# Kernel optimization log

Measured on AMD Instinct MI355X. Metric: run time of the kernel, lower is better.

## Reference

```python
import jax, jax.numpy as jnp
import numpy as np

B, NPG = 128, 512            # graphs, nodes per graph (batch is contiguous & uniform)
N = B * NPG                  # 65536 nodes
DEG = 8
E = N * DEG                  # 524288 edges
F_IN, NHID = 128, 64
H, C = 3, NHID               # GAT heads, out channels per head
HC = H * C                   # 192
NCLS = 10
RATIO = 0.5
NEG_SLOPE = 0.2


def setup_inputs() -> dict:
    key = jax.random.key(0)
    ks = jax.random.split(key, 24)
    x = jax.random.normal(ks[0], (N, F_IN), jnp.float32)
    # edges constrained within each graph (graphs are contiguous blocks of NPG nodes)
    offs = jnp.repeat(jnp.arange(B, dtype=jnp.int32) * NPG, NPG * DEG)
    src = jax.random.randint(ks[1], (E,), 0, NPG, dtype=jnp.int32) + offs
    dst = jax.random.randint(ks[2], (E,), 0, NPG, dtype=jnp.int32) + offs
    edge_index = jnp.stack([src, dst], axis=0)
    edge_attr = jax.random.normal(ks[3], (E, 2), jnp.float32)
    batch = jnp.repeat(jnp.arange(B, dtype=jnp.int32), NPG)

    def lin(k, o, i):
        return jax.random.normal(k, (o, i), jnp.float32) / np.float32(np.sqrt(i))

    return {
        "x": x, "edge_index": edge_index, "edge_attr": edge_attr, "batch": batch,
        # lin: num_features -> nhid//2
        "W_lin": lin(ks[4], NHID // 2, F_IN), "b_lin": jnp.zeros((NHID // 2,), jnp.float32),
        # GATConv(nhid//2 -> nhid, heads=3, edge_dim=2)
        "W_src": lin(ks[5], HC, NHID // 2),
        "att_src": jax.random.normal(ks[6], (H, C), jnp.float32) / np.float32(np.sqrt(C)),
        "att_dst": jax.random.normal(ks[7], (H, C), jnp.float32) / np.float32(np.sqrt(C)),
        "W_edge": lin(ks[8], HC, 2),
        "att_edge": jax.random.normal(ks[9], (H, C), jnp.float32) / np.float32(np.sqrt(C)),
        "b_gat": jnp.zeros((HC,), jnp.float32),
        # SAGPool score layer: GCNConv(nhid*3 -> 1)
        "W_gcn": lin(ks[10], 1, HC), "b_gcn": jnp.zeros((1,), jnp.float32),
        # classifier MLP
        "W1": lin(ks[11], NHID, 2 * HC), "b1": jnp.zeros((NHID,), jnp.float32),
        "W2": lin(ks[12], NHID // 2, NHID), "b2": jnp.zeros((NHID // 2,), jnp.float32),
        "W3": lin(ks[13], NCLS, NHID // 2), "b3": jnp.zeros((NCLS,), jnp.float32),
    }


def reference(x, edge_index, edge_attr, batch,
              W_lin, b_lin, W_src, att_src, att_dst, W_edge, att_edge, b_gat,
              W_gcn, b_gcn, W1, b1, W2, b2, W3, b3):
    src, dst = edge_index[0], edge_index[1]

    # ---- lin + ELU -------------------------------------------------------
    h = jax.nn.elu(x @ W_lin.T + b_lin)                       # [N, nhid//2]

    # ---- GATConv(heads=3, edge_dim=2), add_self_loops fill_value='mean' --
    loop = jnp.arange(N, dtype=src.dtype)
    cnt = jax.ops.segment_sum(jnp.ones((E,), h.dtype), dst, num_segments=N)
    loop_attr = jax.ops.segment_sum(edge_attr, dst, num_segments=N) / jnp.maximum(cnt, 1.0)[:, None]
    s_full = jnp.concatenate([src, loop])
    d_full = jnp.concatenate([dst, loop])
    ea_full = jnp.concatenate([edge_attr, loop_attr], axis=0)  # [E+N, 2]

    xp = (h @ W_src.T).reshape(N, H, C)                        # projected per-head feats
    a_src = (xp * att_src).sum(-1)                             # [N, H]
    a_dst = (xp * att_dst).sum(-1)                             # [N, H]
    ef = (ea_full @ W_edge.T).reshape(-1, H, C)
    a_edge = (ef * att_edge).sum(-1)                           # [E+N, H]

    alpha = jax.nn.leaky_relu(a_src[s_full] + a_dst[d_full] + a_edge, NEG_SLOPE)
    m = jax.ops.segment_max(alpha, d_full, num_segments=N)     # scatter-softmax over dst
    ealpha = jnp.exp(alpha - m[d_full])
    denom = jax.ops.segment_sum(ealpha, d_full, num_segments=N)
    alpha = ealpha / (denom[d_full] + 1e-16)                   # [E+N, H]

    out = jax.ops.segment_sum(alpha[:, :, None] * xp[s_full], d_full, num_segments=N)
    x1 = jax.nn.relu(out.reshape(N, HC) + b_gat)               # [N, 192]

    # ---- SAGPool: GCNConv score + per-graph top-k (mask form) ------------
    xw = x1 @ W_gcn.T                                          # [N, 1]
    deg = jax.ops.segment_sum(jnp.ones((E,), x1.dtype), dst, num_segments=N) + 1.0
    dinv = jax.lax.rsqrt(deg)
    agg = jax.ops.segment_sum((dinv[src] * dinv[dst])[:, None] * xw[src], dst, num_segments=N)
    score = (agg + (dinv ** 2)[:, None] * xw + b_gcn)[:, 0]    # [N]

    k = int(np.ceil(RATIO * NPG))                              # nodes kept per graph
    s2 = score.reshape(B, NPG)
    rank = jnp.argsort(jnp.argsort(-s2, axis=1), axis=1)
    mask = rank < k                                            # [B, NPG] top-k selection

    xs = (x1 * jnp.tanh(score)[:, None]).reshape(B, NPG, HC)
    gmp = jnp.max(jnp.where(mask[:, :, None], xs, -jnp.inf), axis=1)   # [B, 192]
    gap = jnp.sum(jnp.where(mask[:, :, None], xs, 0.0), axis=1) / k    # [B, 192]
    r = jnp.concatenate([gmp, gap], axis=1)                    # [B, 384]

    # ---- classifier MLP (dropout is identity in eval) ---------------------
    r = jax.nn.relu(r @ W1.T + b1)
    r = jax.nn.relu(r @ W2.T + b2)
    return jax.nn.log_softmax(r @ W3.T + b3, axis=-1)          # [B, num_classes]
```

## Files before the change

kernel.cpp:

```cpp
#include <hip/hip_runtime.h>
#include <hip/hip_bf16.h>
#include <math.h>

#define NN   65536
#define EE   524288
#define BB   128
#define NPGC 512
#define HCC  192
#define KSEL 256
#define NEG  0.2f
#define PSEG 8
#define SEGN (NPGC / PSEG)
#define MAXD 40
#define SLOTS ((size_t)NN * MAXD)
#define EPG   4096

__device__ __forceinline__ int nodeblock_base(int bx) {
    int xcd = bx & 7, j = bx >> 3;
    int g = xcd + 8 * (j >> 1);
    return g * NPGC + (j & 1) * 256;
}

__global__ __launch_bounds__(192) void k_v(
    const float* __restrict__ W_src, const float* __restrict__ att_src,
    const float* __restrict__ att_dst, const float* __restrict__ W_edge,
    const float* __restrict__ att_edge, float* __restrict__ vbuf) {
    __shared__ float red[6];
    int t = threadIdx.x;
    if (t < 6) red[t] = 0.f;
    __syncthreads();
    {
        float ae = att_edge[t];
        int h = t >> 6;
        atomicAdd(&red[h],     W_edge[2 * t]     * ae);
        atomicAdd(&red[3 + h], W_edge[2 * t + 1] * ae);
    }
    if (t < 96) {
        int h = t >> 5, k = t & 31;
        float vs = 0.f, vd = 0.f;
        for (int c = 0; c < 64; ++c) {
            float w = W_src[(h * 64 + c) * 32 + k];
            vs += w * att_src[h * 64 + c];
            vd += w * att_dst[h * 64 + c];
        }
        vbuf[t] = vs;
        vbuf[96 + t] = vd;
    }
    __syncthreads();
    if (t < 6) vbuf[192 + t] = red[t];
}

__global__ __launch_bounds__(256) void k_h(
    const float* __restrict__ x, const float* __restrict__ W_lin,
    const float* __restrict__ b_lin, const float* __restrict__ vbuf,
    float* __restrict__ hbuf, float* __restrict__ ap_s, float* __restrict__ ap_d) {
    __shared__ float Wl[128 * 16];
    __shared__ float vs_s[48], vd_s[48];
    int t = threadIdx.x;
    int half = blockIdx.y;
#pragma unroll
    for (int i = 0; i < 8; ++i) {
        int idx = t + i * 256;
        int k = idx >> 4, jj = idx & 15;
        Wl[k * 16 + jj] = W_lin[(half * 16 + jj) * 128 + k];
    }
    if (t < 48) {
        int head = t >> 4, j = t & 15;
        vs_s[t] = vbuf[head * 32 + half * 16 + j];
        vd_s[t] = vbuf[96 + head * 32 + half * 16 + j];
    }
    __syncthreads();
    int g = (blockIdx.x & 7) + 8 * (blockIdx.x >> 3);
    int nA = g * NPGC + t, nB = nA + 256;
    const float4* xrA = (const float4*)(x + (size_t)nA * 128);
    const float4* xrB = (const float4*)(x + (size_t)nB * 128);
    float accA[16], accB[16];
#pragma unroll
    for (int j = 0; j < 16; ++j) {
        float bv = b_lin[half * 16 + j];
        accA[j] = bv; accB[j] = bv;
    }
#pragma unroll 2
    for (int q = 0; q < 32; ++q) {
        float4 xA = xrA[q], xB = xrB[q];
        const float4* w0 = (const float4*)&Wl[(q * 4 + 0) * 16];
        const float4* w1 = (const float4*)&Wl[(q * 4 + 1) * 16];
        const float4* w2 = (const float4*)&Wl[(q * 4 + 2) * 16];
        const float4* w3 = (const float4*)&Wl[(q * 4 + 3) * 16];
#pragma unroll
        for (int jq = 0; jq < 4; ++jq) {
            float4 a = w0[jq], b = w1[jq], c = w2[jq], d = w3[jq];
            accA[4*jq+0] += xA.x*a.x + xA.y*b.x + xA.z*c.x + xA.w*d.x;
            accA[4*jq+1] += xA.x*a.y + xA.y*b.y + xA.z*c.y + xA.w*d.y;
            accA[4*jq+2] += xA.x*a.z + xA.y*b.z + xA.z*c.z + xA.w*d.z;
            accA[4*jq+3] += xA.x*a.w + xA.y*b.w + xA.z*c.w + xA.w*d.w;
            accB[4*jq+0] += xB.x*a.x + xB.y*b.x + xB.z*c.x + xB.w*d.x;
            accB[4*jq+1] += xB.x*a.y + xB.y*b.y + xB.z*c.y + xB.w*d.y;
            accB[4*jq+2] += xB.x*a.z + xB.y*b.z + xB.z*c.z + xB.w*d.z;
            accB[4*jq+3] += xB.x*a.w + xB.y*b.w + xB.z*c.w + xB.w*d.w;
        }
    }
#pragma unroll
    for (int j = 0; j < 16; ++j) {
        accA[j] = accA[j] > 0.f ? accA[j] : expm1f(accA[j]);
        accB[j] = accB[j] > 0.f ? accB[j] : expm1f(accB[j]);
    }
    float4* dA = (float4*)(hbuf + (size_t)nA * 32 + half * 16);
    float4* dB = (float4*)(hbuf + (size_t)nB * 32 + half * 16);
#pragma unroll
    for (int q = 0; q < 4; ++q) {
        dA[q] = make_float4(accA[4*q], accA[4*q+1], accA[4*q+2], accA[4*q+3]);
        dB[q] = make_float4(accB[4*q], accB[4*q+1], accB[4*q+2], accB[4*q+3]);
    }
#pragma unroll
    for (int head = 0; head < 3; ++head) {
        float sA = 0.f, dAv = 0.f, sB = 0.f, dBv = 0.f;
#pragma unroll
        for (int j = 0; j < 16; ++j) {
            sA  += accA[j] * vs_s[head * 16 + j];
            dAv += accA[j] * vd_s[head * 16 + j];
            sB  += accB[j] * vs_s[head * 16 + j];
            dBv += accB[j] * vd_s[head * 16 + j];
        }
        size_t pb = (size_t)(half * 3 + head) * NN;
        ap_s[pb + nA] = sA;  ap_s[pb + nB] = sB;
        ap_d[pb + nA] = dAv; ap_d[pb + nB] = dBv;
    }
}

__global__ __launch_bounds__(256) void k_xp(
    const float* __restrict__ hbuf, const float* __restrict__ W_src,
    float* __restrict__ xp) {
    __shared__ float hs[256 * 32];
    int t = threadIdx.x;
    int nb = nodeblock_base(blockIdx.x);
    for (int i = t; i < 256 * 32; i += 256) hs[i] = hbuf[(size_t)nb * 32 + i];
    int lane = t & 63, wave = t >> 6;
    float wreg[96];
#pragma unroll
    for (int h = 0; h < 3; ++h) {
        const float4* wp = (const float4*)(W_src + (h * 64 + lane) * 32);
#pragma unroll
        for (int q = 0; q < 8; ++q) {
            float4 w = wp[q];
            wreg[h * 32 + 4 * q]     = w.x;
            wreg[h * 32 + 4 * q + 1] = w.y;
            wreg[h * 32 + 4 * q + 2] = w.z;
            wreg[h * 32 + 4 * q + 3] = w.w;
        }
    }
    __syncthreads();
    int n0 = wave * 64;
    for (int nd = 0; nd < 64; ++nd) {
        int nl = n0 + nd;
        const float4* hr = (const float4*)&hs[nl * 32];
        float a0 = 0.f, a1 = 0.f, a2 = 0.f;
#pragma unroll
        for (int q = 0; q < 8; ++q) {
            float4 hv = hr[q];
            a0 += hv.x*wreg[4*q] + hv.y*wreg[4*q+1] + hv.z*wreg[4*q+2] + hv.w*wreg[4*q+3];
            a1 += hv.x*wreg[32+4*q] + hv.y*wreg[32+4*q+1] + hv.z*wreg[32+4*q+2] + hv.w*wreg[32+4*q+3];
            a2 += hv.x*wreg[64+4*q] + hv.y*wreg[64+4*q+1] + hv.z*wreg[64+4*q+2] + hv.w*wreg[64+4*q+3];
        }
        size_t nbase = (size_t)(nb + nl) * HCC;
        xp[nbase + lane] = a0;
        xp[nbase + 64 + lane] = a1;
        xp[nbase + 128 + lane] = a2;
    }
}

__global__ __launch_bounds__(1024) void k_edges(
    const int* __restrict__ ei, const float* __restrict__ ea,
    const float* __restrict__ ap_s, const float* __restrict__ ap_d,
    const float* __restrict__ vbuf,
    int* __restrict__ fill, float4* __restrict__ slotA) {
    __shared__ int   s_pos[NPGC];
    __shared__ float s_la[NPGC * 2];
    __shared__ float s_as[NPGC * 3], s_ad[NPGC * 3];
    int b = blockIdx.x, t = threadIdx.x;
    int g = (b & 7) + 8 * (b >> 3);
    int nbase = g * NPGC;
    int ebase = g * EPG;
    if (t < NPGC) s_pos[t] = 0;
    s_la[t] = 0.f;
    for (int i = t; i < NPGC * 3; i += 1024) {
        int h = i >> 9, nl = i & (NPGC - 1);
        s_as[nl * 3 + h] = ap_s[(size_t)h * NN + nbase + nl] +
                           ap_s[(size_t)(3 + h) * NN + nbase + nl];
        s_ad[nl * 3 + h] = ap_d[(size_t)h * NN + nbase + nl] +
                           ap_d[(size_t)(3 + h) * NN + nbase + nl];
    }
    float ac[6];
#pragma unroll
    for (int h = 0; h < 6; ++h) ac[h] = vbuf[192 + h];
    int4  se  = ((const int4*)(ei + ebase))[t];
    int4  de  = ((const int4*)(ei + EE + ebase))[t];
    float4 a0 = ((const float4*)(ea + 2 * ebase))[2 * t];
    float4 a1 = ((const float4*)(ea + 2 * ebase))[2 * t + 1];
    __syncthreads();

    int   ss[4] = {se.x, se.y, se.z, se.w};
    int   dd[4] = {de.x, de.y, de.z, de.w};
    float e0v[4] = {a0.x, a0.z, a1.x, a1.z};
    float e1v[4] = {a0.y, a0.w, a1.y, a1.w};
#pragma unroll
    for (int k = 0; k < 4; ++k) {
        int s = ss[k], d = dd[k];
        int sl = s & (NPGC - 1), dl = d & (NPGC - 1);
        float e0 = e0v[k], e1 = e1v[k];
        atomicAdd(&s_la[2 * dl],     e0);
        atomicAdd(&s_la[2 * dl + 1], e1);
        float v[3];
#pragma unroll
        for (int h = 0; h < 3; ++h) {
            float a = s_as[sl * 3 + h] + s_ad[dl * 3 + h] +
                      e0 * ac[h] + e1 * ac[3 + h];
            v[h] = a >= 0.f ? a : NEG * a;
        }
        int pos = atomicAdd(&s_pos[dl], 1);
        if (pos < MAXD - 1)
            slotA[(size_t)(nbase + dl) * MAXD + 1 + pos] =
                make_float4(v[0], v[1], v[2], __int_as_float(s));
    }
    __syncthreads();
    if (t < NPGC) {
        int cnt = s_pos[t];
        int n = nbase + t;
        fill[n] = cnt;
        float inv = 1.f / fmaxf((float)cnt, 1.f);
        float l0 = s_la[2 * t] * inv, l1 = s_la[2 * t + 1] * inv;
        float v[3];
#pragma unroll
        for (int h = 0; h < 3; ++h) {
            float a = s_as[t * 3 + h] + s_ad[t * 3 + h] +
                      l0 * ac[h] + l1 * ac[3 + h];
            v[h] = a >= 0.f ? a : NEG * a;
        }
        slotA[(size_t)n * MAXD] = make_float4(v[0], v[1], v[2],
                                              __int_as_float(n));
    }
}

__global__ __launch_bounds__(256) void k_agg(
    const int* __restrict__ fill, const float4* __restrict__ slotA,
    const float* __restrict__ xp,
    const float* __restrict__ b_gat, const float* __restrict__ W_gcn,
    float* __restrict__ x1, float* __restrict__ xwd, float* __restrict__ dinv) {
    __shared__ float2 wsl[4][3][65];
    int wave = threadIdx.x >> 6, lane = threadIdx.x & 63;
    int b = blockIdx.x;
    int xcd = b & 7, j = b >> 3;
    int g = (j >> 7) * 8 + xcd;
    int n = g * NPGC + (j & 127) * 4 + wave;

    int ctrue = fill[n];
    int cnt = ctrue < (MAXD - 1) ? ctrue : (MAXD - 1);
    int tot = cnt + 1;

    if (lane < tot) {
        float4 pk = slotA[(size_t)n * MAXD + lane];
        wsl[wave][0][lane] = make_float2(__expf(pk.x), pk.w);
        wsl[wave][1][lane] = make_float2(__expf(pk.y), pk.w);
        wsl[wave][2][lane] = make_float2(__expf(pk.z), pk.w);
    }
    bool act = lane < 48;
    int head = act ? (lane >> 4) : 0;
    const float2* wp = &wsl[wave][head][0];
    const float4* xp4 = (const float4*)xp;
    float ax = 0.f, ay = 0.f, az = 0.f, aw = 0.f, den = 0.f;
    int s = 0;
    for (; s + 3 < tot; s += 4) {
        float2 wsA = wp[s],     wsB = wp[s + 1];
        float2 wsC = wp[s + 2], wsD = wp[s + 3];
        den += (wsA.x + wsB.x) + (wsC.x + wsD.x);
        if (act) {
            float4 vA = xp4[(size_t)__float_as_int(wsA.y) * 48 + lane];
            float4 vB = xp4[(size_t)__float_as_int(wsB.y) * 48 + lane];
            float4 vC = xp4[(size_t)__float_as_int(wsC.y) * 48 + lane];
            float4 vD = xp4[(size_t)__float_as_int(wsD.y) * 48 + lane];
            ax += wsA.x * vA.x + wsB.x * vB.x + wsC.x * vC.x + wsD.x * vD.x;
            ay += wsA.x * vA.y + wsB.x * vB.y + wsC.x * vC.y + wsD.x * vD.y;
            az += wsA.x * vA.z + wsB.x * vB.z + wsC.x * vC.z + wsD.x * vD.z;
            aw += wsA.x * vA.w + wsB.x * vB.w + wsC.x * vC.w + wsD.x * vD.w;
        }
    }
    for (; s < tot; ++s) {
        float2 wsA = wp[s];
        den += wsA.x;
        if (act) {
            float4 vA = xp4[(size_t)__float_as_int(wsA.y) * 48 + lane];
            ax += wsA.x * vA.x; ay += wsA.x * vA.y;
            az += wsA.x * vA.z; aw += wsA.x * vA.w;
        }
    }
    float p = 0.f;
    if (act) {
        float id = 1.f / (den + 1e-16f);
        float4 bg = ((const float4*)b_gat)[lane];
        float4 v;
        v.x = fmaxf(ax * id + bg.x, 0.f);
        v.y = fmaxf(ay * id + bg.y, 0.f);
        v.z = fmaxf(az * id + bg.z, 0.f);
        v.w = fmaxf(aw * id + bg.w, 0.f);
        ((float4*)x1)[(size_t)n * 48 + lane] = v;
        float4 wg = ((const float4*)W_gcn)[lane];
        p = v.x * wg.x + v.y * wg.y + v.z * wg.z + v.w * wg.w;
    }
#pragma unroll
    for (int msk = 32; msk > 0; msk >>= 1) p += __shfl_xor(p, msk, 64);
    if (lane == 0) {
        float dv = rsqrtf((float)ctrue + 1.f);
        xwd[n] = p * dv;
        dinv[n] = dv;
    }
}

__global__ __launch_bounds__(256) void k_score(
    const int* __restrict__ fill, const float4* __restrict__ slotA,
    const float* __restrict__ xwd, const float* __restrict__ dinv,
    const float* __restrict__ b_gcn, float* __restrict__ score) {
    int wave = threadIdx.x >> 6, lane = threadIdx.x & 63;
    int b = blockIdx.x;
    int xcd = b & 7, j = b >> 3;
    int g = (j >> 7) * 8 + xcd;
    int n = g * NPGC + (j & 127) * 4 + wave;

    int ctrue = fill[n];
    int cnt = ctrue < (MAXD - 1) ? ctrue : (MAXD - 1);
    float acc = 0.f;
    if (lane <= cnt) {
        int src = __float_as_int(
            ((const float*)slotA)[((size_t)n * MAXD + lane) * 4 + 3]);
        acc = xwd[src];
    }
#pragma unroll
    for (int msk = 32; msk > 0; msk >>= 1) acc += __shfl_xor(acc, msk, 64);
    if (lane == 0) score[n] = b_gcn[0] + dinv[n] * acc;
}

__global__ __launch_bounds__(192) void k_poolrank(
    const float* __restrict__ score, const float* __restrict__ x1,
    float* __restrict__ pmax, float* __restrict__ psum) {
    __shared__ float sc[NPGC];
    __shared__ float ts_s[SEGN];
    __shared__ int sel_s[SEGN];
    int b = blockIdx.x;
    int xcd = b & 7, gslot = (b >> 3) & 15, seg = b >> 7;
    int g = gslot * 8 + xcd;
    int t = threadIdx.x;
    int gbase = g * NPGC;
    for (int i = t; i < NPGC; i += 192) sc[i] = score[gbase + i];
    __syncthreads();
    if (t < SEGN) {
        int iloc = seg * SEGN + t;
        float si = sc[iloc];
        int rank = 0;
        for (int j = 0; j < NPGC; ++j) {
            float sj = sc[j];
            rank += (sj > si) || (sj == si && j < iloc);
        }
        sel_s[t] = (rank < KSEL) ? 1 : 0;
        ts_s[t] = tanhf(si);
    }
    __syncthreads();
    int nb = gbase + seg * SEGN;
    float mx = -1e30f, sm = 0.f;
    for (int i = 0; i < SEGN; ++i) {
        if (sel_s[i]) {
            float v = x1[(size_t)(nb + i) * HCC + t] * ts_s[i];
            mx = fmaxf(mx, v);
            sm += v;
        }
    }
    size_t pb = (size_t)(g * PSEG + seg) * HCC + t;
    pmax[pb] = mx;
    psum[pb] = sm;
}

__global__ __launch_bounds__(384) void k_mlp(
    const float* __restrict__ pmax, const float* __restrict__ psum,
    const float* __restrict__ W1, const float* __restrict__ b1,
    const float* __restrict__ W2, const float* __restrict__ b2,
    const float* __restrict__ W3, const float* __restrict__ b3,
    float* __restrict__ out) {
    __shared__ float rs[384], part[384], h1[64], h2[32], lg[10], mls;
    int g = blockIdx.x, t = threadIdx.x;
    if (t < HCC) {
        float mx = -1e30f, sm = 0.f;
#pragma unroll
        for (int s = 0; s < PSEG; ++s) {
            mx = fmaxf(mx, pmax[(size_t)(g * PSEG + s) * HCC + t]);
            sm += psum[(size_t)(g * PSEG + s) * HCC + t];
        }
        rs[t] = mx;
        rs[HCC + t] = sm * (1.f / (float)KSEL);
    }
    __syncthreads();
    {
        int o = t / 6, sl = t - o * 6;
        const float* wr = W1 + o * 384 + sl * 64;
        const float* rr = rs + sl * 64;
        float s = 0.f;
#pragma unroll 8
        for (int k = 0; k < 64; ++k) s += rr[k] * wr[k];
        part[t] = s;
    }
    __syncthreads();
    if (t < 64) {
        float s = b1[t];
#pragma unroll
        for (int j = 0; j < 6; ++j) s += part[t * 6 + j];
        h1[t] = fmaxf(s, 0.f);
    }
    __syncthreads();
    if (t < 256) {
        int o = t >> 3, sl = t & 7;
        const float* wr = W2 + o * 64 + sl * 8;
        const float* hr = h1 + sl * 8;
        float s = 0.f;
#pragma unroll
        for (int k = 0; k < 8; ++k) s += hr[k] * wr[k];
        part[t] = s;
    }
    __syncthreads();
    if (t < 32) {
        float s = b2[t];
#pragma unroll
        for (int j = 0; j < 8; ++j) s += part[t * 8 + j];
        h2[t] = fmaxf(s, 0.f);
    }
    __syncthreads();
    if (t < 10) {
        float s = b3[t];
        for (int k = 0; k < 32; ++k) s += h2[k] * W3[t * 32 + k];
        lg[t] = s;
    }
    __syncthreads();
    if (t == 0) {
        float mx = lg[0];
        for (int j = 1; j < 10; ++j) mx = fmaxf(mx, lg[j]);
        float se = 0.f;
        for (int j = 0; j < 10; ++j) se += expf(lg[j] - mx);
        mls = mx + logf(se);
    }
    __syncthreads();
    if (t < 10) out[g * 10 + t] = lg[t] - mls;
}

extern "C" void kernel_launch(void* const* d_in, const int* in_sizes, int n_in,
                              void* d_out, int out_size, void* d_ws, size_t ws_size,
                              hipStream_t stream) {
    const float* x        = (const float*)d_in[0];
    const int*   ei       = (const int*)d_in[1];
    const float* ea       = (const float*)d_in[2];
    const float* W_lin    = (const float*)d_in[4];
    const float* b_lin    = (const float*)d_in[5];
    const float* W_src    = (const float*)d_in[6];
    const float* att_src  = (const float*)d_in[7];
    const float* att_dst  = (const float*)d_in[8];
    const float* W_edge   = (const float*)d_in[9];
    const float* att_edge = (const float*)d_in[10];
    const float* b_gat    = (const float*)d_in[11];
    const float* W_gcn    = (const float*)d_in[12];
    const float* b_gcn    = (const float*)d_in[13];
    const float* W1 = (const float*)d_in[14]; const float* b1 = (const float*)d_in[15];
    const float* W2 = (const float*)d_in[16]; const float* b2 = (const float*)d_in[17];
    const float* W3 = (const float*)d_in[18]; const float* b3 = (const float*)d_in[19];
    float* out = (float*)d_out;

    char* ws = (char*)d_ws;
    size_t off = 0;
    auto alloc = [&](size_t bytes) {
        size_t r = off;
        off += (bytes + 255) & ~(size_t)255;
        return r;
    };
    float* xp      = (float*)(ws + alloc((size_t)NN * HCC * 4));
    float* x1      = (float*)(ws + alloc((size_t)NN * HCC * 4));
    float* hbuf    = (float*)(ws + alloc((size_t)NN * 32 * 4));
    int*   fill    = (int*)(ws + alloc((size_t)NN * 4));
    float* ap_s    = (float*)(ws + alloc((size_t)NN * 6 * 4));
    float* ap_d    = (float*)(ws + alloc((size_t)NN * 6 * 4));
    float4* slotA  = (float4*)(ws + alloc(SLOTS * 16));
    float* xwd     = (float*)(ws + alloc((size_t)NN * 4));
    float* dinv    = (float*)(ws + alloc((size_t)NN * 4));
    float* score   = (float*)(ws + alloc((size_t)NN * 4));
    float* vbuf    = (float*)(ws + alloc(256 * 4));
    float* pmax    = (float*)(ws + alloc((size_t)BB * PSEG * HCC * 4));
    float* psum    = (float*)(ws + alloc((size_t)BB * PSEG * HCC * 4));

    k_v<<<1, 192, 0, stream>>>(W_src, att_src, att_dst, W_edge, att_edge, vbuf);
    k_h<<<dim3(128, 2), 256, 0, stream>>>(x, W_lin, b_lin, vbuf,
                                          hbuf, ap_s, ap_d);
    k_xp<<<256, 256, 0, stream>>>(hbuf, W_src, xp);
    k_edges<<<BB, 1024, 0, stream>>>(ei, ea, ap_s, ap_d, vbuf, fill, slotA);
    k_agg<<<NN / 4, 256, 0, stream>>>(fill, slotA, xp, b_gat, W_gcn,
                                      x1, xwd, dinv);
    k_score<<<NN / 4, 256, 0, stream>>>(fill, slotA, xwd, dinv, b_gcn, score);
    k_poolrank<<<BB * PSEG, 192, 0, stream>>>(score, x1, pmax, psum);
    k_mlp<<<BB, 384, 0, stream>>>(pmax, psum, W1, b1, W2, b2, W3, b3, out);
}
```

Measured before the change: 263.7 us.

## Fuse input linear layer with GAT source projection in one kernel

```diff
diff --git a/kernel.cpp b/kernel.cpp
--- a/kernel.cpp
+++ b/kernel.cpp
@@ -9,11 +9,12 @@
 #define HCC  192
 #define KSEL 256
 #define NEG  0.2f
-#define PSEG 8
+#define PSEG 16
 #define SEGN (NPGC / PSEG)
 #define MAXD 40
 #define SLOTS ((size_t)NN * MAXD)
 #define EPG   4096
+#define HSTR  36
 
 __device__ __forceinline__ int nodeblock_base(int bx) {
     int xcd = bx & 7, j = bx >> 3;
@@ -50,91 +51,57 @@
     if (t < 6) vbuf[192 + t] = red[t];
 }
 
-__global__ __launch_bounds__(256) void k_h(
+__global__ __launch_bounds__(256) void k_feat(
     const float* __restrict__ x, const float* __restrict__ W_lin,
-    const float* __restrict__ b_lin, const float* __restrict__ vbuf,
-    float* __restrict__ hbuf, float* __restrict__ ap_s, float* __restrict__ ap_d) {
-    __shared__ float Wl[128 * 16];
-    __shared__ float vs_s[48], vd_s[48];
+    const float* __restrict__ b_lin, const float* __restrict__ W_src,
+    const float* __restrict__ vbuf,
+    float* __restrict__ xp, float* __restrict__ ap_s, float* __restrict__ ap_d) {
+    __shared__ float Wl[128 * HSTR];
+    __shared__ float hs[256 * HSTR];
+    __shared__ float vs_s[96], vd_s[96];
     int t = threadIdx.x;
-    int half = blockIdx.y;
-#pragma unroll
-    for (int i = 0; i < 8; ++i) {
-        int idx = t + i * 256;
-        int k = idx >> 4, jj = idx & 15;
-        Wl[k * 16 + jj] = W_lin[(half * 16 + jj) * 128 + k];
-    }
-    if (t < 48) {
-        int head = t >> 4, j = t & 15;
-        vs_s[t] = vbuf[head * 32 + half * 16 + j];
-        vd_s[t] = vbuf[96 + head * 32 + half * 16 + j];
-    }
-    __syncthreads();
-    int g = (blockIdx.x & 7) + 8 * (blockIdx.x >> 3);
-    int nA = g * NPGC + t, nB = nA + 256;
-    const float4* xrA = (const float4*)(x + (size_t)nA * 128);
-    const float4* xrB = (const float4*)(x + (size_t)nB * 128);
-    float accA[16], accB[16];
-#pragma unroll
-    for (int j = 0; j < 16; ++j) {
-        float bv = b_lin[half * 16 + j];
-        accA[j] = bv; accB[j] = bv;
-    }
+    for (int i = t; i < 4096; i += 256) {
+        int j = i >> 7, k = i & 127;
+        Wl[k * HSTR + j] = W_lin[i];
+    }
+    if (t < 96) { vs_s[t] = vbuf[t]; vd_s[t] = vbuf[96 + t]; }
+    __syncthreads();
+    int nb = nodeblock_base(blockIdx.x);
+    int n = nb + t;
+    const float4* xr = (const float4*)(x + (size_t)n * 128);
+    float acc[32];
+#pragma unroll
+    for (int j = 0; j < 32; ++j) acc[j] = b_lin[j];
 #pragma unroll 2
     for (int q = 0; q < 32; ++q) {
-        float4 xA = xrA[q], xB = xrB[q];
-        const float4* w0 = (const float4*)&Wl[(q * 4 + 0) * 16];
-        const float4* w1 = (const float4*)&Wl[(q * 4 + 1) * 16];
-        const float4* w2 = (const float4*)&Wl[(q * 4 + 2) * 16];
-        const float4* w3 = (const float4*)&Wl[(q * 4 + 3) * 16];
-#pragma unroll
-        for (int jq = 0; jq < 4; ++jq) {
-            float4 a = w0[jq], b = w1[jq], c = w2[jq], d = w3[jq];
-            accA[4*jq+0] += xA.x*a.x + xA.y*b.x + xA.z*c.x + xA.w*d.x;
-            accA[4*jq+1] += xA.x*a.y + xA.y*b.y + xA.z*c.y + xA.w*d.y;
-            accA[4*jq+2] += xA.x*a.z + xA.y*b.z + xA.z*c.z + xA.w*d.z;
-            accA[4*jq+3] += xA.x*a.w + xA.y*b.w + xA.z*c.w + xA.w*d.w;
-            accB[4*jq+0] += xB.x*a.x + xB.y*b.x + xB.z*c.x + xB.w*d.x;
-            accB[4*jq+1] += xB.x*a.y + xB.y*b.y + xB.z*c.y + xB.w*d.y;
-            accB[4*jq+2] += xB.x*a.z + xB.y*b.z + xB.z*c.z + xB.w*d.z;
-            accB[4*jq+3] += xB.x*a.w + xB.y*b.w + xB.z*c.w + xB.w*d.w;
-        }
-    }
-#pragma unroll
-    for (int j = 0; j < 16; ++j) {
-        accA[j] = accA[j] > 0.f ? accA[j] : expm1f(accA[j]);
-        accB[j] = accB[j] > 0.f ? accB[j] : expm1f(accB[j]);
-    }
-    float4* dA = (float4*)(hbuf + (size_t)nA * 32 + half * 16);
-    float4* dB = (float4*)(hbuf + (size_t)nB * 32 + half * 16);
-#pragma unroll
-    for (int q = 0; q < 4; ++q) {
-        dA[q] = make_float4(accA[4*q], accA[4*q+1], accA[4*q+2], accA[4*q+3]);
-        dB[q] = make_float4(accB[4*q], accB[4*q+1], accB[4*q+2], accB[4*q+3]);
-    }
+        float4 a = xr[q];
+        const float* w = &Wl[(q * 4) * HSTR];
+#pragma unroll
+        for (int j = 0; j < 32; ++j) {
+            acc[j] += a.x * w[j] + a.y * w[HSTR + j] +
+                      a.z * w[2 * HSTR + j] + a.w * w[3 * HSTR + j];
+        }
+    }
+#pragma unroll
+    for (int j = 0; j < 32; ++j)
+        acc[j] = acc[j] > 0.f ? acc[j] : expm1f(acc[j]);
 #pragma unroll
     for (int head = 0; head < 3; ++head) {
-        float sA = 0.f, dAv = 0.f, sB = 0.f, dBv = 0.f;
-#pragma unroll
-        for (int j = 0; j < 16; ++j) {
-            sA  += accA[j] * vs_s[head * 16 + j];
-            dAv += accA[j] * vd_s[head * 16 + j];
-            sB  += accB[j] * vs_s[head * 16 + j];
-            dBv += accB[j] * vd_s[head * 16 + j];
-        }
-        size_t pb = (size_t)(half * 3 + head) * NN;
-        ap_s[pb + nA] = sA;  ap_s[pb + nB] = sB;
-        ap_d[pb + nA] = dAv; ap_d[pb + nB] = dBv;
-    }
-}
-
-__global__ __launch_bounds__(256) void k_xp(
-    const float* __restrict__ hbuf, const float* __restrict__ W_src,
-    float* __restrict__ xp) {
-    __shared__ float hs[256 * 32];
-    int t = threadIdx.x;
-    int nb = nodeblock_base(blockIdx.x);
-    for (int i = t; i < 256 * 32; i += 256) hs[i] = hbuf[(size_t)nb * 32 + i];
+        float s = 0.f, d = 0.f;
+#pragma unroll
+        for (int j = 0; j < 32; ++j) {
+            s += acc[j] * vs_s[head * 32 + j];
+            d += acc[j] * vd_s[head * 32 + j];
+        }
+        ap_s[(size_t)head * NN + n] = s;
+        ap_d[(size_t)head * NN + n] = d;
+    }
+    float4* hw = (float4*)&hs[t * HSTR];
+#pragma unroll
+    for (int q = 0; q < 8; ++q)
+        hw[q] = make_float4(acc[4 * q], acc[4 * q + 1],
+                            acc[4 * q + 2], acc[4 * q + 3]);
+    __syncthreads();
     int lane = t & 63, wave = t >> 6;
     float wreg[96];
 #pragma unroll
@@ -149,11 +116,10 @@
             wreg[h * 32 + 4 * q + 3] = w.w;
         }
     }
-    __syncthreads();
     int n0 = wave * 64;
     for (int nd = 0; nd < 64; ++nd) {
         int nl = n0 + nd;
-        const float4* hr = (const float4*)&hs[nl * 32];
+        const float4* hr = (const float4*)&hs[nl * HSTR];
         float a0 = 0.f, a1 = 0.f, a2 = 0.f;
 #pragma unroll
         for (int q = 0; q < 8; ++q) {
@@ -185,10 +151,8 @@
     s_la[t] = 0.f;
     for (int i = t; i < NPGC * 3; i += 1024) {
         int h = i >> 9, nl = i & (NPGC - 1);
-        s_as[nl * 3 + h] = ap_s[(size_t)h * NN + nbase + nl] +
-                           ap_s[(size_t)(3 + h) * NN + nbase + nl];
-        s_ad[nl * 3 + h] = ap_d[(size_t)h * NN + nbase + nl] +
-                           ap_d[(size_t)(3 + h) * NN + nbase + nl];
+        s_as[nl * 3 + h] = ap_s[(size_t)h * NN + nbase + nl];
+        s_ad[nl * 3 + h] = ap_d[(size_t)h * NN + nbase + nl];
     }
     float ac[6];
 #pragma unroll
@@ -477,10 +441,9 @@
     };
     float* xp      = (float*)(ws + alloc((size_t)NN * HCC * 4));
     float* x1      = (float*)(ws + alloc((size_t)NN * HCC * 4));
-    float* hbuf    = (float*)(ws + alloc((size_t)NN * 32 * 4));
     int*   fill    = (int*)(ws + alloc((size_t)NN * 4));
-    float* ap_s    = (float*)(ws + alloc((size_t)NN * 6 * 4));
-    float* ap_d    = (float*)(ws + alloc((size_t)NN * 6 * 4));
+    float* ap_s    = (float*)(ws + alloc((size_t)NN * 3 * 4));
+    float* ap_d    = (float*)(ws + alloc((size_t)NN * 3 * 4));
     float4* slotA  = (float4*)(ws + alloc(SLOTS * 16));
     float* xwd     = (float*)(ws + alloc((size_t)NN * 4));
     float* dinv    = (float*)(ws + alloc((size_t)NN * 4));
@@ -490,9 +453,8 @@
     float* psum    = (float*)(ws + alloc((size_t)BB * PSEG * HCC * 4));
 
     k_v<<<1, 192, 0, stream>>>(W_src, att_src, att_dst, W_edge, att_edge, vbuf);
-    k_h<<<dim3(128, 2), 256, 0, stream>>>(x, W_lin, b_lin, vbuf,
-                                          hbuf, ap_s, ap_d);
-    k_xp<<<256, 256, 0, stream>>>(hbuf, W_src, xp);
+    k_feat<<<256, 256, 0, stream>>>(x, W_lin, b_lin, W_src, vbuf,
+                                    xp, ap_s, ap_d);
     k_edges<<<BB, 1024, 0, stream>>>(ei, ea, ap_s, ap_d, vbuf, fill, slotA);
     k_agg<<<NN / 4, 256, 0, stream>>>(fill, slotA, xp, b_gat, W_gcn,
                                       x1, xwd, dinv);
```

Measured after the change: 253.0 us. 1.04x faster.
